# Optimization experiments

Hardware: AMD Instinct MI355X
Metric: run time of the kernel (lower is better)

Reference implementation:

```python
import jax, jax.numpy as jnp
import numpy as np

EPS = 1e-5
TEMP = 0.2  # contrastive temperature


def setup_inputs() -> dict:
    key = jax.random.key(0)
    ks_ = jax.random.split(key, 16)
    N, d, d_free, D, F_ = 10000, 32, 32, 64, 3
    x = jax.random.normal(ks_[0], (N, 256), dtype=jnp.float32)
    feats = jax.random.normal(ks_[1], (F_, N, d), dtype=jnp.float32)
    feat_free = 0.01 * jax.random.normal(ks_[2], (N, d_free), dtype=jnp.float32)
    # curvatures: k = init_curvature * randn(); keep away from 0 so the curved branch is taken
    ks = jax.random.uniform(ks_[3], (F_,), dtype=jnp.float32) + 0.5
    Ws = jax.random.normal(ks_[4], (F_, D, d), dtype=jnp.float32)
    Ws = Ws / jnp.linalg.norm(Ws, axis=-1, keepdims=True)  # row-normalized as in __init__
    bias = 2.0 * jnp.pi * jax.random.uniform(ks_[5], (F_, D), dtype=jnp.float32)
    W_free = jax.random.normal(ks_[6], (D, d_free), dtype=jnp.float32)
    W_free = W_free / jnp.linalg.norm(W_free, axis=-1, keepdims=True)
    b_free = 2.0 * jnp.pi * jax.random.uniform(ks_[7], (D,), dtype=jnp.float32)
    W1 = 0.05 * jax.random.normal(ks_[8], (3 * d, 64), dtype=jnp.float32)
    b1 = jnp.zeros((64,), dtype=jnp.float32)
    W2 = 0.05 * jax.random.normal(ks_[9], (64, 1), dtype=jnp.float32)
    b2 = jnp.zeros((1,), dtype=jnp.float32)
    motif = jax.random.randint(ks_[10], (3, 50000), 0, N, dtype=jnp.int32)
    neg_uv = jax.random.randint(ks_[11], (2, 50000), 0, N, dtype=jnp.int32)
    return {"x": x, "feats": feats, "feat_free": feat_free, "ks": ks,
            "Ws": Ws, "bias": bias, "W_free": W_free, "b_free": b_free,
            "W1": W1, "b1": b1, "W2": W2, "b2": b2,
            "motif": motif, "neg_uv": neg_uv}


def _normalize(xf, k):
    # RiemannianFeatures.normalize with the random scale fixed at 0.5 for determinism
    radius = 1.0 / jnp.sqrt(jnp.abs(k))
    xn = jnp.linalg.norm(xf, axis=-1, keepdims=True)
    return xf / xn * (0.9 * 0.5) * radius


def _mlp(f3, W1, b1, W2, b2):
    return jax.nn.relu(f3 @ W1 + b1) @ W2 + b2  # [M, 1]


def _gather3(feat, m):
    # nodes_from_motif: concat features of u, v, w
    return jnp.concatenate([feat[m[0]], feat[m[1]], feat[m[2]]], axis=-1)


def reference(x, feats, feat_free, ks, Ws, bias, W_free, b_free,
              W1, b1, W2, b2, motif, neg_uv):
    F_, N, d = feats.shape
    d_free = feat_free.shape[-1]

    # ---- RiemannianFeatures.forward: normalized products per factor + free part
    products = [_normalize(feats[i], ks[i]) for i in range(F_)]
    products.append(feat_free)

    # ---- random_mapping: pairwise manifold distance -> exp/cos transform
    zs = []
    for i in range(F_):
        xi, w, b, k = products[i], Ws[i], bias[i], ks[i]
        div = jnp.sum((xi[:, None, :] - w[None, :, :]) ** 2, axis=-1)      # [N, D]
        num = 1.0 + k * jnp.sum(xi * xi, axis=-1, keepdims=True)           # [N, 1]
        dist = jnp.log(num / (div + EPS))
        zs.append(jnp.exp((d - 1) * dist * 0.5) * jnp.cos(dist + b))
    dist_f = feat_free @ W_free.T                                          # Euclidean branch
    zs.append(jnp.exp((d_free - 1) * dist_f * 0.5) * jnp.cos(dist_f + b_free))
    x2 = jnp.concatenate(zs, axis=-1)                                      # [N, embed]

    # ---- cal_cl_loss: full N x N cosine-similarity contrastive loss
    n1 = jnp.linalg.norm(x, axis=-1)
    n2 = jnp.linalg.norm(x2, axis=-1)
    sim = jnp.einsum('ik,jk->ij', x, x2) / (n1[:, None] * n2[None, :])
    sim = jnp.exp(sim / TEMP)
    pos = jnp.diagonal(sim)
    loss_1 = -jnp.mean(jnp.log(pos / (jnp.sum(sim, axis=0) - pos)))
    loss_2 = -jnp.mean(jnp.log(pos / (jnp.sum(sim, axis=1) - pos)))
    cl_loss = 0.5 * (loss_1 + loss_2)

    # ---- cal_motif_loss: gather triples -> MLP -> BCE (neg via provided sampled pairs)
    neg_motif = jnp.concatenate([neg_uv, motif[2:3]], axis=0)
    motif_loss = jnp.float32(0.0)
    for p in products:
        pos_logit = _mlp(_gather3(p, motif), W1, b1, W2, b2)
        neg_logit = _mlp(_gather3(p, neg_motif), W1, b1, W2, b2)
        motif_loss = motif_loss \
            - jnp.mean(jax.nn.log_sigmoid(pos_logit)) \
            - jnp.mean(jax.nn.log_sigmoid(-neg_logit))

    return cl_loss + motif_loss
```

## Files before the change

kernel.cpp:

```cpp
#include <hip/hip_runtime.h>
#include <hip/hip_bf16.h>
#include <math.h>

#define EMBED 256
#define NF 3
#define DD 64
#define BM 128
#define BN 128
#define BKF 128
#define MOTIF_BLOCKS 2048

typedef unsigned short ushort_t;
typedef unsigned char uchar_t;
typedef float f32x4 __attribute__((ext_vector_type(4)));
typedef float f32x2 __attribute__((ext_vector_type(2)));

__device__ __forceinline__ void gl2lds16(const void* g, void* l) {
    __builtin_amdgcn_global_load_lds(
        (const __attribute__((address_space(1))) unsigned int*)g,
        (__attribute__((address_space(3))) unsigned int*)l, 16, 0, 0);
}

__device__ __forceinline__ uchar_t f2fp8(float f) {
    int p = __builtin_amdgcn_cvt_pk_fp8_f32(f, f, 0, false);
    return (uchar_t)(p & 0xff);
}
template<bool HI>
__device__ __forceinline__ f32x2 pk2(unsigned int w) {
    return __builtin_amdgcn_cvt_pk_f32_fp8((int)w, HI);
}

__global__ __launch_bounds__(256) void k_embed(
    const float* __restrict__ x,
    const float* __restrict__ feats,
    const float* __restrict__ feat_free,
    const float* __restrict__ ks,
    const float* __restrict__ Ws,
    const float* __restrict__ bias,
    const float* __restrict__ W_free,
    const float* __restrict__ b_free,
    float* __restrict__ p_out,
    uchar_t* __restrict__ xnf8,
    uchar_t* __restrict__ x2nf8,
    float* __restrict__ zero_base,
    int N, int Npad)
{
    int wave = threadIdx.x >> 6;
    int t    = threadIdx.x & 63;
    int n = blockIdx.x * 4 + wave;
    int gid = blockIdx.x * 256 + threadIdx.x;
    if (gid < 2*N) zero_base[gid] = 0.f;

    __shared__ float Wl[128*65];
    __shared__ float xi_s[4][NF][32];
    __shared__ float ff_s[4][32];

    for (int e = threadIdx.x; e < NF*DD*32; e += 256) {
        int i = e >> 11, rem = e & 2047, tr = rem >> 5, c = rem & 31;
        Wl[(i*32 + c)*65 + tr] = Ws[e];
    }
    for (int e = threadIdx.x; e < DD*32; e += 256) {
        int tr = e >> 5, c = e & 31;
        Wl[(96 + c)*65 + tr] = W_free[e];
    }

    bool active = (n < N);
    if (!active && n < Npad) {
        ((int*)(xnf8  + (size_t)n*EMBED))[t] = 0;
        ((int*)(x2nf8 + (size_t)n*EMBED))[t] = 0;
    }

    float (*xi)[32] = xi_s[wave];
    float* ffs = ff_s[wave];

    float v[NF];
    float ffv = 0.f;
    if (active && t < 32) {
        #pragma unroll
        for (int i = 0; i < NF; ++i) v[i] = feats[((size_t)i*N + n)*32 + t];
        ffv = feat_free[(size_t)n*32 + t];
    } else {
        #pragma unroll
        for (int i = 0; i < NF; ++i) v[i] = 0.f;
    }

    float num[NF];
    #pragma unroll
    for (int i = 0; i < NF; ++i) {
        float s = v[i]*v[i];
        s += __shfl_xor(s, 1, 64);  s += __shfl_xor(s, 2, 64);
        s += __shfl_xor(s, 4, 64);  s += __shfl_xor(s, 8, 64);
        s += __shfl_xor(s, 16, 64);
        s = __shfl(s, 0, 64);
        float k = ks[i];
        float scale = 0.45f / (sqrtf(s) * sqrtf(fabsf(k)));
        float xv = v[i] * scale;
        if (active && t < 32) {
            xi[i][t] = xv;
            p_out[((size_t)i*N + n)*32 + t] = xv;
        }
        num[i] = 1.0f + k * (scale*scale*s);
    }
    if (active && t < 32) ffs[t] = ffv;
    __syncthreads();
    if (!active) return;

    float z[4];
    float zsq = 0.f;
    #pragma unroll
    for (int i = 0; i < NF; ++i) {
        float div = 0.f;
        #pragma unroll
        for (int c = 0; c < 32; ++c) {
            float d = xi[i][c] - Wl[(i*32 + c)*65 + t];
            div += d*d;
        }
        float dist = __logf(num[i] / (div + 1e-5f));
        float zz = __expf(15.5f * dist) * __cosf(dist + bias[i*DD + t]);
        z[i] = zz;
        zsq += zz*zz;
    }
    {
        float dot = 0.f;
        #pragma unroll
        for (int c = 0; c < 32; ++c) dot = fmaf(ffs[c], Wl[(96 + c)*65 + t], dot);
        float zz = __expf(15.5f * dot) * __cosf(dot + b_free[t]);
        z[3] = zz;
        zsq += zz*zz;
    }
    zsq += __shfl_xor(zsq, 1, 64);  zsq += __shfl_xor(zsq, 2, 64);
    zsq += __shfl_xor(zsq, 4, 64);  zsq += __shfl_xor(zsq, 8, 64);
    zsq += __shfl_xor(zsq, 16, 64); zsq += __shfl_xor(zsq, 32, 64);
    float iv2 = 1.0f / sqrtf(zsq);

    #pragma unroll
    for (int i = 0; i < NF; ++i) x2nf8[(size_t)n*EMBED + i*DD + t] = f2fp8(z[i]*iv2);
    x2nf8[(size_t)n*EMBED + 192 + t] = f2fp8(z[3]*iv2);

    float xv[4];
    float s1 = 0.f;
    #pragma unroll
    for (int q = 0; q < 4; ++q) { xv[q] = x[(size_t)n*EMBED + q*64 + t]; s1 += xv[q]*xv[q]; }
    s1 += __shfl_xor(s1, 1, 64);  s1 += __shfl_xor(s1, 2, 64);
    s1 += __shfl_xor(s1, 4, 64);  s1 += __shfl_xor(s1, 8, 64);
    s1 += __shfl_xor(s1, 16, 64); s1 += __shfl_xor(s1, 32, 64);
    float iv1 = 1.0f / sqrtf(s1);
    #pragma unroll
    for (int q = 0; q < 4; ++q) xnf8[(size_t)n*EMBED + q*64 + t] = f2fp8(xv[q]*iv1);
}

__global__ __launch_bounds__(256) void k_mlp1(
    const float* __restrict__ p,
    const float* __restrict__ feat_free,
    const float* __restrict__ W1,
    const float* __restrict__ b1,
    uchar_t* __restrict__ H,
    int N)
{
    int lane = threadIdx.x & 63;
    int gw = (blockIdx.x * blockDim.x + threadIdx.x) >> 6;
    int nwaves = (gridDim.x * blockDim.x) >> 6;

    float wcol[96];
    #pragma unroll
    for (int c = 0; c < 96; ++c) wcol[c] = W1[c*64 + lane];
    float b1l = b1[lane];

    int total = 4 * N;
    for (int unit = gw; unit < total; unit += nwaves) {
        int node = __builtin_amdgcn_readfirstlane(unit >> 2);
        int prod = __builtin_amdgcn_readfirstlane(unit & 3);
        const float* P = (prod < 3) ? (p + ((size_t)prod*N + node)*32)
                                    : (feat_free + (size_t)node*32);
        float fc[32];
        #pragma unroll
        for (int c = 0; c < 32; ++c) fc[c] = P[c];
        #pragma unroll
        for (int s = 0; s < 3; ++s) {
            float h = (s == 2) ? b1l : 0.f;
            #pragma unroll
            for (int c = 0; c < 32; ++c) h = fmaf(fc[c], wcol[s*32 + c], h);
            H[(((size_t)prod*3 + s)*N + node)*64 + lane] = f2fp8(h);
        }
    }
}

__global__ __launch_bounds__(256) void k_motif3(
    const uchar_t* __restrict__ H,
    const int* __restrict__ motif,
    const int* __restrict__ neg_uv,
    const float* __restrict__ W2,
    const float* __restrict__ b2,
    float* __restrict__ partials,
    int N, int M)
{
    int lane = threadIdx.x & 63;
    int sub  = lane >> 3;
    int ch   = (lane & 7) * 8;
    int caseId = blockIdx.x & 7;
    int rank   = (blockIdx.x >> 3) * 4 + (threadIdx.x >> 6);
    int prod  = caseId >> 1;
    int isneg = caseId & 1;
    const uchar_t* Hu = H + ((size_t)prod*3 + 0)*N*64;
    const uchar_t* Hv = H + ((size_t)prod*3 + 1)*N*64;
    const uchar_t* Hw = H + ((size_t)prod*3 + 2)*N*64;
    const int* iu = isneg ? neg_uv       : motif;
    const int* iv = isneg ? (neg_uv + M) : (motif + M);
    const int* iw = motif + 2*M;

    float w2c[8];
    #pragma unroll
    for (int c = 0; c < 8; ++c) w2c[c] = W2[ch + c];
    float b2v = b2[0];

    float accl = 0.f;
    #pragma unroll 2
    for (int r0 = rank*8; r0 < M; r0 += 8192) {
        int r = r0 + sub;
        bool ok = (r < M);
        int rc = ok ? r : 0;
        int u = iu[rc], v = iv[rc], w = iw[rc];
        uint2 du = *(const uint2*)&Hu[(size_t)u*64 + ch];
        uint2 dv = *(const uint2*)&Hv[(size_t)v*64 + ch];
        uint2 dw = *(const uint2*)&Hw[(size_t)w*64 + ch];
        float pl = 0.f;
        {
            f32x2 s;
            s = pk2<false>(du.x) + pk2<false>(dv.x) + pk2<false>(dw.x);
            pl = fmaf(fmaxf(s.x,0.f), w2c[0], pl);  pl = fmaf(fmaxf(s.y,0.f), w2c[1], pl);
            s = pk2<true>(du.x) + pk2<true>(dv.x) + pk2<true>(dw.x);
            pl = fmaf(fmaxf(s.x,0.f), w2c[2], pl);  pl = fmaf(fmaxf(s.y,0.f), w2c[3], pl);
            s = pk2<false>(du.y) + pk2<false>(dv.y) + pk2<false>(dw.y);
            pl = fmaf(fmaxf(s.x,0.f), w2c[4], pl);  pl = fmaf(fmaxf(s.y,0.f), w2c[5], pl);
            s = pk2<true>(du.y) + pk2<true>(dv.y) + pk2<true>(dw.y);
            pl = fmaf(fmaxf(s.x,0.f), w2c[6], pl);  pl = fmaf(fmaxf(s.y,0.f), w2c[7], pl);
        }
        pl += __shfl_xor(pl, 1, 64);
        pl += __shfl_xor(pl, 2, 64);
        pl += __shfl_xor(pl, 4, 64);
        float logit = pl + b2v;
        float z = isneg ? -logit : logit;
        float sp = fmaxf(-z, 0.f) + __logf(1.f + __expf(-fabsf(z)));
        accl -= ok ? sp : 0.f;
    }
    #pragma unroll
    for (int m = 1; m < 64; m <<= 1) accl += __shfl_xor(accl, m, 64);

    __shared__ float wred[4];
    if (lane == 0) wred[threadIdx.x >> 6] = accl;
    __syncthreads();
    if (threadIdx.x == 0)
        partials[blockIdx.x] = (wred[0] + wred[1] + wred[2] + wred[3]) * 0.125f;
}

__global__ __launch_bounds__(256) void k_sim(
    const uchar_t* __restrict__ xn, const uchar_t* __restrict__ x2n,
    float* __restrict__ rowsum, float* __restrict__ colsum, float* __restrict__ pos,
    int N, int nb, int nbr, int roff)
{
    __shared__ __align__(16) uchar_t As[BM*BKF];
    __shared__ __align__(16) uchar_t Bs[BN*BKF];
    __shared__ float rsum_s[BM];
    __shared__ float csum_s[BN];

    int tid  = threadIdx.x;
    int lane = tid & 63;
    int w    = tid >> 6;
    int wr   = w >> 1, wc = w & 1;
    int quad = lane >> 4, l15 = lane & 15;

    int pid = blockIdx.x;
    int per_group = 8 * nb;
    int group = pid / per_group;
    int rem = pid - group * per_group;
    int rowspan = min(8, nbr - group * 8);
    int prow = roff + group * 8 + rem % rowspan;
    int pcol = rem / rowspan;
    int row0 = prow * BM, col0 = pcol * BN;

    if (tid < BM) { rsum_s[tid] = 0.f; csum_s[tid] = 0.f; }

    f32x4 acc[4][4];
    #pragma unroll
    for (int i = 0; i < 4; ++i)
        #pragma unroll
        for (int j = 0; j < 4; ++j) acc[i][j] = (f32x4){0.f,0.f,0.f,0.f};

    for (int kt = 0; kt < EMBED; kt += BKF) {
        #pragma unroll
        for (int i = 0; i < 4; ++i) {
            int slot = i*256 + tid;
            int r = slot >> 3, c = slot & 7;
            int sc = c ^ (r & 7);
            gl2lds16(xn  + (size_t)(row0 + r)*EMBED + kt + sc*16, &As[slot*16]);
            gl2lds16(x2n + (size_t)(col0 + r)*EMBED + kt + sc*16, &Bs[slot*16]);
        }
        __syncthreads();
        #pragma unroll
        for (int s = 0; s < 4; ++s) {
            long a[4], b[4];
            int g = s*2 + (quad >> 1);
            int sub8 = (quad & 1) * 8;
            #pragma unroll
            for (int ti = 0; ti < 4; ++ti) {
                int ra = wr*64 + ti*16 + l15;
                a[ti] = *(const long*)&As[ra*BKF + (g ^ (ra & 7))*16 + sub8];
            }
            #pragma unroll
            for (int tj = 0; tj < 4; ++tj) {
                int rb = wc*64 + tj*16 + l15;
                b[tj] = *(const long*)&Bs[rb*BKF + (g ^ (rb & 7))*16 + sub8];
            }
            #pragma unroll
            for (int ti = 0; ti < 4; ++ti)
                #pragma unroll
                for (int tj = 0; tj < 4; ++tj)
                    acc[ti][tj] = __builtin_amdgcn_mfma_f32_16x16x32_fp8_fp8(a[ti], b[tj], acc[ti][tj], 0, 0, 0);
        }
        __syncthreads();
    }

    #pragma unroll
    for (int ti = 0; ti < 4; ++ti) {
        #pragma unroll
        for (int tj = 0; tj < 4; ++tj) {
            #pragma unroll
            for (int r = 0; r < 4; ++r) {
                int gi = row0 + wr*64 + ti*16 + quad*4 + r;
                int gj = col0 + wc*64 + tj*16 + l15;
                float e = 0.f;
                if (gi < N && gj < N) {
                    e = __expf(acc[ti][tj][r] * 5.0f);
                    if (gi == gj) pos[gi] = e;
                }
                acc[ti][tj][r] = e;
            }
        }
    }
    #pragma unroll
    for (int ti = 0; ti < 4; ++ti) {
        #pragma unroll
        for (int r = 0; r < 4; ++r) {
            float rsv = acc[ti][0][r] + acc[ti][1][r] + acc[ti][2][r] + acc[ti][3][r];
            rsv += __shfl_xor(rsv, 1, 64);
            rsv += __shfl_xor(rsv, 2, 64);
            rsv += __shfl_xor(rsv, 4, 64);
            rsv += __shfl_xor(rsv, 8, 64);
            if (l15 == 0) atomicAdd(&rsum_s[wr*64 + ti*16 + quad*4 + r], rsv);
        }
    }
    #pragma unroll
    for (int tj = 0; tj < 4; ++tj) {
        float csv = 0.f;
        #pragma unroll
        for (int ti = 0; ti < 4; ++ti)
            #pragma unroll
            for (int r = 0; r < 4; ++r) csv += acc[ti][tj][r];
        csv += __shfl_xor(csv, 16, 64);
        csv += __shfl_xor(csv, 32, 64);
        if (lane < 16) atomicAdd(&csum_s[wc*64 + tj*16 + lane], csv);
    }
    __syncthreads();
    if (tid < BM) {
        int gi = row0 + tid;
        if (gi < N) atomicAdd(&rowsum[gi], rsum_s[tid]);
        int gj = col0 + tid;
        if (gj < N) atomicAdd(&colsum[gj], csum_s[tid]);
    }
}

__global__ __launch_bounds__(256) void k_final(
    const float* __restrict__ rowsum, const float* __restrict__ colsum,
    const float* __restrict__ pos, const float* __restrict__ partials,
    float* __restrict__ out, int N, int M, int nparts)
{
    __shared__ float red1[256], red2[256], red3[256];
    int t = threadIdx.x;
    float l1 = 0.f, l2 = 0.f, mo = 0.f;
    for (int i = t; i < N; i += 256) {
        float pv = pos[i];
        l1 += __logf((colsum[i] - pv) / pv);
        l2 += __logf((rowsum[i] - pv) / pv);
    }
    for (int i = t; i < nparts; i += 256) mo += partials[i];
    red1[t] = l1; red2[t] = l2; red3[t] = mo; __syncthreads();
    for (int s = 128; s > 0; s >>= 1) {
        if (t < s) { red1[t] += red1[t+s]; red2[t] += red2[t+s]; red3[t] += red3[t+s]; }
        __syncthreads();
    }
    if (t == 0) {
        float cl = 0.5f * (red1[0] + red2[0]) / (float)N;
        out[0] = cl - red3[0] / (float)M;
    }
}

extern "C" void kernel_launch(void* const* d_in, const int* in_sizes, int n_in,
                              void* d_out, int out_size, void* d_ws, size_t ws_size,
                              hipStream_t stream)
{
    const float* x         = (const float*)d_in[0];
    const float* feats     = (const float*)d_in[1];
    const float* feat_free = (const float*)d_in[2];
    const float* ks        = (const float*)d_in[3];
    const float* Ws        = (const float*)d_in[4];
    const float* bias      = (const float*)d_in[5];
    const float* W_free    = (const float*)d_in[6];
    const float* b_free    = (const float*)d_in[7];
    const float* W1        = (const float*)d_in[8];
    const float* b1        = (const float*)d_in[9];
    const float* W2        = (const float*)d_in[10];
    const float* b2        = (const float*)d_in[11];
    const int*   motif     = (const int*)d_in[12];
    const int*   neg_uv    = (const int*)d_in[13];
    int N = in_sizes[0] / EMBED;
    int M = in_sizes[13] / 2;
    int nb = (N + BM - 1) / BM;
    int Npad = nb * BM;

    uchar_t* xnf8  = (uchar_t*)d_ws;
    uchar_t* x2nf8 = xnf8 + (size_t)Npad*EMBED;
    uchar_t* H8    = x2nf8 + (size_t)Npad*EMBED;
    float* p      = (float*)(H8 + (size_t)12*N*64);
    float* posv   = p + (size_t)3*N*32;
    float* rowsum = posv + N;
    float* colsum = rowsum + N;
    float* partials = colsum + N;

    k_embed<<<(Npad + 3) / 4, 256, 0, stream>>>(x, feats, feat_free, ks, Ws, bias,
                                                W_free, b_free, p, xnf8, x2nf8,
                                                rowsum, N, Npad);
    k_mlp1<<<512, 256, 0, stream>>>(p, feat_free, W1, b1, H8, N);
    k_motif3<<<MOTIF_BLOCKS, 256, 0, stream>>>(H8, motif, neg_uv, W2, b2, partials, N, M);
    int nbr1 = nb / 2, nbr2 = nb - nbr1;
    k_sim<<<nbr1 * nb, 256, 0, stream>>>(xnf8, x2nf8, rowsum, colsum, posv, N, nb, nbr1, 0);
    k_sim<<<nbr2 * nb, 256, 0, stream>>>(xnf8, x2nf8, rowsum, colsum, posv, N, nb, nbr2, nbr1);
    k_final<<<1, 256, 0, stream>>>(rowsum, colsum, posv, partials, (float*)d_out, N, M, MOTIF_BLOCKS);
}
```

Baseline: 266.7 us.

## Fuse first MLP layer into embedding kernel and split similarity into four launches

Computes the per-node first-layer MLP projections inside the embedding kernel from the normalized features already held in shared memory. This removes the separate k_mlp1 launch and the round trip of the normalized product features through global memory. It also folds the 1/temperature scale into the fp8 quantization of x, which removes a multiply in the sim epilogue but changes fp8 rounding and dynamic range. The similarity kernel is now launched as four row chunks instead of two. The fused embedding kernel needs more registers for the 96 weight columns, which may reduce its occupancy.

```diff
diff --git a/kernel.cpp b/kernel.cpp
--- a/kernel.cpp
+++ b/kernel.cpp
@@ -39,9 +39,11 @@
     const float* __restrict__ bias,
     const float* __restrict__ W_free,
     const float* __restrict__ b_free,
-    float* __restrict__ p_out,
+    const float* __restrict__ W1,
+    const float* __restrict__ b1,
     uchar_t* __restrict__ xnf8,
     uchar_t* __restrict__ x2nf8,
+    uchar_t* __restrict__ H,
     float* __restrict__ zero_base,
     int N, int Npad)
 {
@@ -94,11 +96,7 @@
         s = __shfl(s, 0, 64);
         float k = ks[i];
         float scale = 0.45f / (sqrtf(s) * sqrtf(fabsf(k)));
-        float xv = v[i] * scale;
-        if (active && t < 32) {
-            xi[i][t] = xv;
-            p_out[((size_t)i*N + n)*32 + t] = xv;
-        }
+        if (active && t < 32) xi[i][t] = v[i] * scale;
         num[i] = 1.0f + k * (scale*scale*s);
     }
     if (active && t < 32) ffs[t] = ffv;
@@ -144,43 +142,23 @@
     s1 += __shfl_xor(s1, 1, 64);  s1 += __shfl_xor(s1, 2, 64);
     s1 += __shfl_xor(s1, 4, 64);  s1 += __shfl_xor(s1, 8, 64);
     s1 += __shfl_xor(s1, 16, 64); s1 += __shfl_xor(s1, 32, 64);
-    float iv1 = 1.0f / sqrtf(s1);
+    float iv1 = 5.0f / sqrtf(s1);
     #pragma unroll
     for (int q = 0; q < 4; ++q) xnf8[(size_t)n*EMBED + q*64 + t] = f2fp8(xv[q]*iv1);
-}
-
-__global__ __launch_bounds__(256) void k_mlp1(
-    const float* __restrict__ p,
-    const float* __restrict__ feat_free,
-    const float* __restrict__ W1,
-    const float* __restrict__ b1,
-    uchar_t* __restrict__ H,
-    int N)
-{
-    int lane = threadIdx.x & 63;
-    int gw = (blockIdx.x * blockDim.x + threadIdx.x) >> 6;
-    int nwaves = (gridDim.x * blockDim.x) >> 6;
 
     float wcol[96];
     #pragma unroll
-    for (int c = 0; c < 96; ++c) wcol[c] = W1[c*64 + lane];
-    float b1l = b1[lane];
-
-    int total = 4 * N;
-    for (int unit = gw; unit < total; unit += nwaves) {
-        int node = __builtin_amdgcn_readfirstlane(unit >> 2);
-        int prod = __builtin_amdgcn_readfirstlane(unit & 3);
-        const float* P = (prod < 3) ? (p + ((size_t)prod*N + node)*32)
-                                    : (feat_free + (size_t)node*32);
-        float fc[32];
-        #pragma unroll
-        for (int c = 0; c < 32; ++c) fc[c] = P[c];
+    for (int c = 0; c < 96; ++c) wcol[c] = W1[c*64 + t];
+    float b1l = b1[t];
+    #pragma unroll
+    for (int prod = 0; prod < 4; ++prod) {
+        const float* P = (prod < 3) ? xi[prod] : ffs;
         #pragma unroll
         for (int s = 0; s < 3; ++s) {
             float h = (s == 2) ? b1l : 0.f;
             #pragma unroll
-            for (int c = 0; c < 32; ++c) h = fmaf(fc[c], wcol[s*32 + c], h);
-            H[(((size_t)prod*3 + s)*N + node)*64 + lane] = f2fp8(h);
+            for (int c = 0; c < 32; ++c) h = fmaf(P[c], wcol[s*32 + c], h);
+            H[(((size_t)prod*3 + s)*N + n)*64 + t] = f2fp8(h);
         }
     }
 }
@@ -330,7 +308,7 @@
                 int gj = col0 + wc*64 + tj*16 + l15;
                 float e = 0.f;
                 if (gi < N && gj < N) {
-                    e = __expf(acc[ti][tj][r] * 5.0f);
+                    e = __expf(acc[ti][tj][r]);
                     if (gi == gj) pos[gi] = e;
                 }
                 acc[ti][tj][r] = e;
@@ -420,19 +398,21 @@
     uchar_t* xnf8  = (uchar_t*)d_ws;
     uchar_t* x2nf8 = xnf8 + (size_t)Npad*EMBED;
     uchar_t* H8    = x2nf8 + (size_t)Npad*EMBED;
-    float* p      = (float*)(H8 + (size_t)12*N*64);
-    float* posv   = p + (size_t)3*N*32;
+    float* posv   = (float*)(H8 + (size_t)12*N*64);
     float* rowsum = posv + N;
     float* colsum = rowsum + N;
     float* partials = colsum + N;
 
     k_embed<<<(Npad + 3) / 4, 256, 0, stream>>>(x, feats, feat_free, ks, Ws, bias,
-                                                W_free, b_free, p, xnf8, x2nf8,
-                                                rowsum, N, Npad);
-    k_mlp1<<<512, 256, 0, stream>>>(p, feat_free, W1, b1, H8, N);
+                                                W_free, b_free, W1, b1,
+                                                xnf8, x2nf8, H8, rowsum, N, Npad);
     k_motif3<<<MOTIF_BLOCKS, 256, 0, stream>>>(H8, motif, neg_uv, W2, b2, partials, N, M);
-    int nbr1 = nb / 2, nbr2 = nb - nbr1;
-    k_sim<<<nbr1 * nb, 256, 0, stream>>>(xnf8, x2nf8, rowsum, colsum, posv, N, nb, nbr1, 0);
-    k_sim<<<nbr2 * nb, 256, 0, stream>>>(xnf8, x2nf8, rowsum, colsum, posv, N, nb, nbr2, nbr1);
+    int q = nb / 4;
+    int off = 0;
+    for (int i = 0; i < 4; ++i) {
+        int nbr = (i == 3) ? (nb - off) : q;
+        k_sim<<<nbr * nb, 256, 0, stream>>>(xnf8, x2nf8, rowsum, colsum, posv, N, nb, nbr, off);
+        off += nbr;
+    }
     k_final<<<1, 256, 0, stream>>>(rowsum, colsum, posv, partials, (float*)d_out, N, M, MOTIF_BLOCKS);
 }
```

Measured after the change: 316.7 us. 1.19x slower.
